# Kernel optimization log

Measured on AMD Instinct MI355X. Metric: run time of the kernel, lower is better.

## Reference

```python
import jax, jax.numpy as jnp
import numpy as np
from itertools import combinations_with_replacement

LATENT_DIM = 16
N_PARAMS = 2
N_VARS = LATENT_DIM + N_PARAMS  # 18
POLY_ORDER = 3
BATCH = 131072

# Static exponent index tables: for each degree d, an [n_terms_d, d] array of
# variable indices (combinations with replacement), matching a sympy-style
# polynomial library [1, x_i, x_i*x_j, x_i*x_j*x_k, ...].
IDX = [np.array(list(combinations_with_replacement(range(N_VARS), d)), dtype=np.int32)
       for d in range(1, POLY_ORDER + 1)]
P = 1 + sum(a.shape[0] for a in IDX)  # 1330 library terms


def setup_inputs() -> dict:
    key = jax.random.key(0)
    k1, k2, k3 = jax.random.split(key, 3)
    z = jax.random.normal(k1, (BATCH, LATENT_DIM), dtype=jnp.float32)
    betas = jax.random.normal(k2, (BATCH, N_PARAMS), dtype=jnp.float32)
    big_xi = jax.random.normal(k3, (P, N_VARS), dtype=jnp.float32) * 0.1
    mask = jnp.ones((P, N_VARS), dtype=jnp.float32)
    return {"z": z, "betas": betas, "big_xi": big_xi, "mask": mask}


def _theta(x):
    # x: [B, N_VARS] -> theta: [B, P]
    cols = [jnp.ones((x.shape[0], 1), dtype=x.dtype)]  # constant term
    for idx in IDX:
        acc = x[:, idx[:, 0]]                # [B, n_terms_d]
        for k in range(1, idx.shape[1]):     # loop over degree (<= POLY_ORDER)
            acc = acc * x[:, idx[:, k]]
        cols.append(acc)
    return jnp.concatenate(cols, axis=1)


def reference(z, betas, big_xi, mask):
    x = jnp.concatenate([z, betas], axis=1)  # [B, N_VARS]
    theta = _theta(x)                        # [B, P]
    return theta @ (big_xi * mask)           # [B, N_VARS]
```

## Files before the change

kernel.cpp:

```cpp
#include <hip/hip_runtime.h>
#include <hip/hip_bf16.h>
#include <utility>


constexpr int NVARS   = 18;
constexpr int NOUT    = 18;
constexpr int NROWS   = 131072;
constexpr int NCHUNKS = 43;
constexpr int NSLOTS  = NCHUNKS * 8;

constexpr int WF0_SHORTS = NCHUNKS * 512;
constexpr int WF1_SHORTS = NCHUNKS * 72;
constexpr int WF_SHORTS  = WF0_SHORTS + WF1_SHORTS;

typedef __attribute__((ext_vector_type(8))) short short8;
typedef __attribute__((ext_vector_type(4))) float f32x4;

struct T3 { int a, b, c; };

constexpr int rho1(int v) {
    if (v < 16)  return (v & ~3) | ((v + 1) & 3);
    if (v == 16) return 17;
    if (v == 17) return 16;
    return v;
}
constexpr int rho2v(int v) { return rho1(rho1(v)); }

constexpr T3 sort3(int u0, int u1, int u2) {
    int t = 0;
    if (u0 > u1) { t = u0; u0 = u1; u1 = t; }
    if (u1 > u2) { t = u1; u1 = u2; u2 = t; }
    if (u0 > u1) { t = u0; u0 = u1; u1 = t; }
    return T3{u0, u1, u2};
}
constexpr T3 rho3(T3 t) { return sort3(rho1(t.a), rho1(t.b), rho1(t.c)); }

constexpr bool t3_less(T3 x, T3 y) {
    if (x.a != y.a) return x.a < y.a;
    if (x.b != y.b) return x.b < y.b;
    return x.c < y.c;
}
constexpr bool t3_eq(T3 x, T3 y) { return x.a == y.a && x.b == y.b && x.c == y.c; }

constexpr int rank_of(T3 t) {
    int deg = (t.a < 18) + (t.b < 18) + (t.c < 18);
    if (deg == 0) return 0;
    if (deg == 1) return 1 + t.a;
    if (deg == 2) {
        int r = 19;
        for (int a = 0; a < t.a; ++a) r += 18 - a;
        return r + (t.b - t.a);
    }
    int r = 190;
    for (int a = 0; a < t.a; ++a) { int n = 18 - a; r += n * (n + 1) / 2; }
    for (int b = t.a; b < t.b; ++b) r += 18 - b;
    return r + (t.c - t.b);
}

struct RepTables {
    signed char va[NSLOTS], vb[NSLOTS], vc[NSLOTS];
    short p[4][NSLOTS];
    int count;
};

constexpr void consider(RepTables& R, int& s, T3 t) {
    T3 im[4] = {t, T3{0, 0, 0}, T3{0, 0, 0}, T3{0, 0, 0}};
    im[1] = rho3(im[0]);
    im[2] = rho3(im[1]);
    im[3] = rho3(im[2]);
    for (int g = 1; g < 4; ++g)
        if (t3_less(im[g], t)) return;
    R.va[s] = (signed char)t.a; R.vb[s] = (signed char)t.b; R.vc[s] = (signed char)t.c;
    for (int g = 0; g < 4; ++g) {
        bool dup = false;
        for (int h = 0; h < g; ++h)
            if (t3_eq(im[h], im[g])) dup = true;
        R.p[g][s] = dup ? (short)-1 : (short)rank_of(im[g]);
    }
    ++s;
}

constexpr RepTables make_tables() {
    RepTables R{};
    int s = 0;
    consider(R, s, T3{18, 18, 18});
    for (int a = 0; a < NVARS; ++a) consider(R, s, T3{a, 18, 18});
    for (int a = 0; a < NVARS; ++a)
        for (int b = a; b < NVARS; ++b) consider(R, s, T3{a, b, 18});
    for (int a = 0; a < NVARS; ++a)
        for (int b = a; b < NVARS; ++b)
            for (int c = b; c < NVARS; ++c) consider(R, s, T3{a, b, c});
    R.count = s;
    for (; s < NSLOTS; ++s) {
        R.va[s] = 19; R.vb[s] = 19; R.vc[s] = 19;
        for (int g = 0; g < 4; ++g) R.p[g][s] = -1;
    }
    return R;
}

constexpr RepTables h_tab = make_tables();
static_assert(h_tab.count == 342, "orbit enumeration must give 342 rep slots");
__device__ const RepTables d_tab = make_tables();

__device__ __align__(16) short g_wf[WF_SHORTS];


#if __has_builtin(__builtin_amdgcn_cvt_pk_bf16_f32)
typedef __bf16 bf16x2 __attribute__((ext_vector_type(2)));
__device__ __forceinline__ unsigned pack2(float f0, float f1) {
    bf16x2 r = __builtin_amdgcn_cvt_pk_bf16_f32(f0, f1);
    return __builtin_bit_cast(unsigned, r);
}
#else
__device__ __forceinline__ unsigned pack2(float f0, float f1) {
    unsigned u0 = __float_as_uint(f0) + 0x8000u;
    unsigned u1 = __float_as_uint(f1) + 0x8000u;
    return __builtin_amdgcn_perm(u1, u0, 0x07060302u);
}
#endif


template <int S>
__device__ __forceinline__ float term_val(const float (&x)[NVARS]) {
    constexpr int a = h_tab.va[S], b = h_tab.vb[S], c = h_tab.vc[S];
    if constexpr (a >= 19)      return 0.0f;
    else if constexpr (a == 18) return 1.0f;
    else if constexpr (b == 18) return x[a];
    else if constexpr (c == 18) return x[a] * x[b];
    else                        return x[a] * x[b] * x[c];
}

union AFrag { unsigned u[4]; short8 v; };

template <int CI, int... I>
__device__ __forceinline__ void eval8(const float (&x)[NVARS], float (&t)[8],
                                      std::integer_sequence<int, I...>) {
    ((t[I] = term_val<CI * 8 + I>(x)), ...);
}

template <int CI>
__device__ __forceinline__ void kstep(const float (&x)[NVARS],
                                      const short* p0, const short* p1,
                                      f32x4& acc0, f32x4& acc1) {
    float t[8];
    eval8<CI>(x, t, std::make_integer_sequence<int, 8>{});
    AFrag af;
#pragma unroll
    for (int j = 0; j < 4; ++j) af.u[j] = pack2(t[2 * j], t[2 * j + 1]);
    short8 b0 = *(const short8*)(p0 + CI * 512);
    short8 b1 = *(const short8*)(p1 + CI * 72);
    acc0 = __builtin_amdgcn_mfma_f32_16x16x32_bf16(af.v, b0, acc0, 0, 0, 0);
    acc1 = __builtin_amdgcn_mfma_f32_16x16x32_bf16(af.v, b1, acc1, 0, 0, 0);
}

template <int... CI>
__device__ __forceinline__ void kloop(const float (&x)[NVARS],
                                      const short* p0, const short* p1,
                                      f32x4& acc0, f32x4& acc1,
                                      std::integer_sequence<int, CI...>) {
    (kstep<CI>(x, p0, p1, acc0, acc1), ...);
}

__device__ __forceinline__ void load_x(const float* __restrict__ z,
                                       const float* __restrict__ betas,
                                       int arow, bool s1, bool s2, float (&x)[NVARS]) {
    float x0[NVARS];
    const float4* z4 = (const float4*)(z + (size_t)arow * 16);
    float4 v0 = z4[0], v1 = z4[1], v2 = z4[2], v3 = z4[3];
    x0[0]  = v0.x; x0[1]  = v0.y; x0[2]  = v0.z; x0[3]  = v0.w;
    x0[4]  = v1.x; x0[5]  = v1.y; x0[6]  = v1.z; x0[7]  = v1.w;
    x0[8]  = v2.x; x0[9]  = v2.y; x0[10] = v2.z; x0[11] = v2.w;
    x0[12] = v3.x; x0[13] = v3.y; x0[14] = v3.z; x0[15] = v3.w;
    const float2 b2 = *(const float2*)(betas + (size_t)arow * 2);
    x0[16] = b2.x; x0[17] = b2.y;
    float y[NVARS];
#pragma unroll
    for (int v = 0; v < NVARS; ++v) y[v] = s1 ? x0[rho1(v)] : x0[v];
#pragma unroll
    for (int v = 0; v < NVARS; ++v) x[v] = s2 ? y[rho2v(v)] : y[v];
}

__global__ __launch_bounds__(512, 4) void vindy_mfma(const float* __restrict__ z,
                                                     const float* __restrict__ betas,
                                                     float* __restrict__ out) {
    __shared__ __align__(16) short ldsW[WF_SHORTS];

    {
        const float4* src = (const float4*)g_wf;
        float4* dst = (float4*)ldsW;
        for (int i = threadIdx.x; i < WF_SHORTS / 8; i += 512) dst[i] = src[i];
    }
    __syncthreads();

    const int lane = threadIdx.x & 63;
    const int wave = threadIdx.x >> 6;
    const int g    = lane >> 4;
    const int n    = lane & 15;
    const int row0 = blockIdx.x * 128 + wave * 16;

    const bool s1 = (g & 1) != 0;
    const bool s2 = (g & 2) != 0;
    float x[NVARS];
    load_x(z, betas, row0 + n, s1, s2, x);

    const short* p0 = ldsW + lane * 8;
    const short* p1 = ldsW + WF0_SHORTS + (n < 2 ? (g * 2 + n) * 8 : 64);

    f32x4 acc0, acc1;
#pragma unroll
    for (int i = 0; i < 4; ++i) { acc0[i] = 0.0f; acc1[i] = 0.0f; }

    kloop(x, p0, p1, acc0, acc1, std::make_integer_sequence<int, NCHUNKS>{});

    float* o = out + (size_t)(row0 + g * 4) * NOUT;
#pragma unroll
    for (int r = 0; r < 4; ++r) o[(size_t)r * NOUT + n] = acc0[r];
    if (n < 2) {
#pragma unroll
        for (int r = 0; r < 4; ++r) o[(size_t)r * NOUT + 16 + n] = acc1[r];
    }
}


__global__ void prep_wfrag(const float* __restrict__ xi, const float* __restrict__ mask) {
    int i = blockIdx.x * blockDim.x + threadIdx.x;
    if (i >= WF_SHORTS) return;
    float v = 0.0f;
    if (i < WF0_SHORTS) {
        int j = i & 7, l = (i >> 3) & 63, c = i >> 9;
        int col = l & 15;
        int p = d_tab.p[l >> 4][c * 8 + j];
        if (p >= 0) v = xi[p * NOUT + col] * mask[p * NOUT + col];
    } else {
        int i2 = i - WF0_SHORTS;
        int c = i2 / 72;
        int r = i2 - c * 72;
        int q = r >> 3, j = r & 7;
        if (q < 8) {
            int col = 16 + (q & 1);
            int p = d_tab.p[q >> 1][c * 8 + j];
            if (p >= 0) v = xi[p * NOUT + col] * mask[p * NOUT + col];
        }
    }
    g_wf[i] = __builtin_bit_cast(short, __float2bfloat16(v));
}

extern "C" void kernel_launch(void* const* d_in, const int* in_sizes, int n_in,
                              void* d_out, int out_size, void* d_ws, size_t ws_size,
                              hipStream_t stream) {
    const float* z     = (const float*)d_in[0];
    const float* betas = (const float*)d_in[1];
    const float* xi    = (const float*)d_in[2];
    const float* mask  = (const float*)d_in[3];
    float* out = (float*)d_out;
    (void)d_ws; (void)ws_size;

    prep_wfrag<<<(WF_SHORTS + 255) / 256, 256, 0, stream>>>(xi, mask);
    vindy_mfma<<<NROWS / 128, 512, 0, stream>>>(z, betas, out);
}
```

Baseline: 89.37 us.

## Switch to 32x32x16 MFMA covering all 18 outputs in one accumulator

Replaces the pair of 16x16x32 MFMAs (one for 16 output columns, one mostly-idle one for the last 2) with a single 32x32x16 MFMA per chunk whose 32 columns cover all 18 outputs. Lanes are split into two halves with a single permutation, and the second orbit permutation is handled by a second pass of 43 chunks over the same rows. The weight fragment layout in LDS is rebuilt with a 304-short chunk stride, and each block now processes 256 rows. The aim is to drop the redundant second MFMA and reuse the term evaluation across more output columns, at the cost of 14 unused columns per MFMA and roughly double the term evaluations per lane.

```diff
diff --git a/kernel.cpp b/kernel.cpp
--- a/kernel.cpp
+++ b/kernel.cpp
@@ -9,12 +9,12 @@
 constexpr int NCHUNKS = 43;
 constexpr int NSLOTS  = NCHUNKS * 8;
 
-constexpr int WF0_SHORTS = NCHUNKS * 512;
-constexpr int WF1_SHORTS = NCHUNKS * 72;
-constexpr int WF_SHORTS  = WF0_SHORTS + WF1_SHORTS;
-
-typedef __attribute__((ext_vector_type(8))) short short8;
-typedef __attribute__((ext_vector_type(4))) float f32x4;
+constexpr int CH_STRIDE = 304;
+constexpr int WF2_SHORTS = 86 * CH_STRIDE;
+constexpr int LDS_SHORTS = 32768;
+
+typedef __attribute__((ext_vector_type(8)))  short short8;
+typedef __attribute__((ext_vector_type(16))) float f32x16;
 
 struct T3 { int a, b, c; };
 
@@ -102,7 +102,7 @@
 static_assert(h_tab.count == 342, "orbit enumeration must give 342 rep slots");
 __device__ const RepTables d_tab = make_tables();
 
-__device__ __align__(16) short g_wf[WF_SHORTS];
+__device__ __align__(16) short g_wf2[WF2_SHORTS];
 
 
 #if __has_builtin(__builtin_amdgcn_cvt_pk_bf16_f32)
@@ -132,38 +132,32 @@
 
 union AFrag { unsigned u[4]; short8 v; };
 
-template <int CI, int... I>
-__device__ __forceinline__ void eval8(const float (&x)[NVARS], float (&t)[8],
-                                      std::integer_sequence<int, I...>) {
-    ((t[I] = term_val<CI * 8 + I>(x)), ...);
+template <int S, int... J>
+__device__ __forceinline__ void pack8(const float (&x)[NVARS], AFrag& af,
+                                      std::integer_sequence<int, J...>) {
+    ((af.u[J] = pack2(term_val<S + 2 * J>(x), term_val<S + 2 * J + 1>(x))), ...);
 }
 
 template <int CI>
-__device__ __forceinline__ void kstep(const float (&x)[NVARS],
-                                      const short* p0, const short* p1,
-                                      f32x4& acc0, f32x4& acc1) {
-    float t[8];
-    eval8<CI>(x, t, std::make_integer_sequence<int, 8>{});
+__device__ __forceinline__ void kstep32(const float (&x)[NVARS],
+                                        const short* pB, f32x16& acc) {
+    constexpr int S = (CI < 43 ? CI : CI - 43) * 8;
     AFrag af;
-#pragma unroll
-    for (int j = 0; j < 4; ++j) af.u[j] = pack2(t[2 * j], t[2 * j + 1]);
-    short8 b0 = *(const short8*)(p0 + CI * 512);
-    short8 b1 = *(const short8*)(p1 + CI * 72);
-    acc0 = __builtin_amdgcn_mfma_f32_16x16x32_bf16(af.v, b0, acc0, 0, 0, 0);
-    acc1 = __builtin_amdgcn_mfma_f32_16x16x32_bf16(af.v, b1, acc1, 0, 0, 0);
-}
-
-template <int... CI>
-__device__ __forceinline__ void kloop(const float (&x)[NVARS],
-                                      const short* p0, const short* p1,
-                                      f32x4& acc0, f32x4& acc1,
-                                      std::integer_sequence<int, CI...>) {
-    (kstep<CI>(x, p0, p1, acc0, acc1), ...);
+    pack8<S>(x, af, std::make_integer_sequence<int, 4>{});
+    short8 b = *(const short8*)(pB + CI * CH_STRIDE);
+    acc = __builtin_amdgcn_mfma_f32_32x32x16_bf16(af.v, b, acc, 0, 0, 0);
+}
+
+template <int BASE, int... CI>
+__device__ __forceinline__ void kloop32(const float (&x)[NVARS],
+                                        const short* pB, f32x16& acc,
+                                        std::integer_sequence<int, CI...>) {
+    (kstep32<BASE + CI>(x, pB, acc), ...);
 }
 
 __device__ __forceinline__ void load_x(const float* __restrict__ z,
                                        const float* __restrict__ betas,
-                                       int arow, bool s1, bool s2, float (&x)[NVARS]) {
+                                       int arow, bool s1, float (&x)[NVARS]) {
     float x0[NVARS];
     const float4* z4 = (const float4*)(z + (size_t)arow * 16);
     float4 v0 = z4[0], v1 = z4[1], v2 = z4[2], v3 = z4[3];
@@ -173,76 +167,75 @@
     x0[12] = v3.x; x0[13] = v3.y; x0[14] = v3.z; x0[15] = v3.w;
     const float2 b2 = *(const float2*)(betas + (size_t)arow * 2);
     x0[16] = b2.x; x0[17] = b2.y;
-    float y[NVARS];
-#pragma unroll
-    for (int v = 0; v < NVARS; ++v) y[v] = s1 ? x0[rho1(v)] : x0[v];
-#pragma unroll
-    for (int v = 0; v < NVARS; ++v) x[v] = s2 ? y[rho2v(v)] : y[v];
+#pragma unroll
+    for (int v = 0; v < NVARS; ++v) x[v] = s1 ? x0[rho1(v)] : x0[v];
 }
 
 __global__ __launch_bounds__(512, 4) void vindy_mfma(const float* __restrict__ z,
                                                      const float* __restrict__ betas,
                                                      float* __restrict__ out) {
-    __shared__ __align__(16) short ldsW[WF_SHORTS];
+    __shared__ __align__(16) short ldsW[LDS_SHORTS];
 
     {
-        const float4* src = (const float4*)g_wf;
+        const float4* src = (const float4*)g_wf2;
         float4* dst = (float4*)ldsW;
-        for (int i = threadIdx.x; i < WF_SHORTS / 8; i += 512) dst[i] = src[i];
+        for (int i = threadIdx.x; i < WF2_SHORTS / 8; i += 512) dst[i] = src[i];
     }
     __syncthreads();
 
     const int lane = threadIdx.x & 63;
     const int wave = threadIdx.x >> 6;
-    const int g    = lane >> 4;
-    const int n    = lane & 15;
-    const int row0 = blockIdx.x * 128 + wave * 16;
-
-    const bool s1 = (g & 1) != 0;
-    const bool s2 = (g & 2) != 0;
-    float x[NVARS];
-    load_x(z, betas, row0 + n, s1, s2, x);
-
-    const short* p0 = ldsW + lane * 8;
-    const short* p1 = ldsW + WF0_SHORTS + (n < 2 ? (g * 2 + n) * 8 : 64);
-
-    f32x4 acc0, acc1;
-#pragma unroll
-    for (int i = 0; i < 4; ++i) { acc0[i] = 0.0f; acc1[i] = 0.0f; }
-
-    kloop(x, p0, p1, acc0, acc1, std::make_integer_sequence<int, NCHUNKS>{});
-
-    float* o = out + (size_t)(row0 + g * 4) * NOUT;
-#pragma unroll
-    for (int r = 0; r < 4; ++r) o[(size_t)r * NOUT + n] = acc0[r];
-    if (n < 2) {
-#pragma unroll
-        for (int r = 0; r < 4; ++r) o[(size_t)r * NOUT + 16 + n] = acc1[r];
+    const int h    = lane >> 5;
+    const int col  = lane & 31;
+    const int row0 = blockIdx.x * 256 + wave * 32;
+
+    float x1[NVARS];
+    load_x(z, betas, row0 + col, h != 0, x1);
+
+    const int col_eff = (col < NOUT) ? col : NOUT;
+    const short* pB = ldsW + h * 152 + col_eff * 8;
+
+    f32x16 acc;
+#pragma unroll
+    for (int i = 0; i < 16; ++i) acc[i] = 0.0f;
+
+    kloop32<0>(x1, pB, acc, std::make_integer_sequence<int, 43>{});
+
+    float x2[NVARS];
+#pragma unroll
+    for (int v = 0; v < NVARS; ++v) x2[v] = x1[rho2v(v)];
+
+    kloop32<43>(x2, pB, acc, std::make_integer_sequence<int, 43>{});
+
+    if (col < NOUT) {
+#pragma unroll
+        for (int q = 0; q < 4; ++q) {
+#pragma unroll
+            for (int r = 0; r < 4; ++r) {
+                int row = r + 8 * q + 4 * h;
+                out[(size_t)(row0 + row) * NOUT + col] = acc[q * 4 + r];
+            }
+        }
     }
 }
 
 
 __global__ void prep_wfrag(const float* __restrict__ xi, const float* __restrict__ mask) {
     int i = blockIdx.x * blockDim.x + threadIdx.x;
-    if (i >= WF_SHORTS) return;
+    if (i >= WF2_SHORTS) return;
+    int c  = i / CH_STRIDE;
+    int r  = i - c * CH_STRIDE;
+    int h  = r / 152;
+    int r2 = r - h * 152;
+    int col = r2 >> 3, j = r2 & 7;
     float v = 0.0f;
-    if (i < WF0_SHORTS) {
-        int j = i & 7, l = (i >> 3) & 63, c = i >> 9;
-        int col = l & 15;
-        int p = d_tab.p[l >> 4][c * 8 + j];
+    if (col < NOUT) {
+        int g = (c < 43 ? 0 : 2) + h;
+        int s = (c < 43 ? c : c - 43) * 8 + j;
+        int p = d_tab.p[g][s];
         if (p >= 0) v = xi[p * NOUT + col] * mask[p * NOUT + col];
-    } else {
-        int i2 = i - WF0_SHORTS;
-        int c = i2 / 72;
-        int r = i2 - c * 72;
-        int q = r >> 3, j = r & 7;
-        if (q < 8) {
-            int col = 16 + (q & 1);
-            int p = d_tab.p[q >> 1][c * 8 + j];
-            if (p >= 0) v = xi[p * NOUT + col] * mask[p * NOUT + col];
-        }
-    }
-    g_wf[i] = __builtin_bit_cast(short, __float2bfloat16(v));
+    }
+    g_wf2[i] = __builtin_bit_cast(short, __float2bfloat16(v));
 }
 
 extern "C" void kernel_launch(void* const* d_in, const int* in_sizes, int n_in,
@@ -255,6 +248,6 @@
     float* out = (float*)d_out;
     (void)d_ws; (void)ws_size;
 
-    prep_wfrag<<<(WF_SHORTS + 255) / 256, 256, 0, stream>>>(xi, mask);
-    vindy_mfma<<<NROWS / 128, 512, 0, stream>>>(z, betas, out);
-}
+    prep_wfrag<<<(WF2_SHORTS + 255) / 256, 256, 0, stream>>>(xi, mask);
+    vindy_mfma<<<NROWS / 256, 512, 0, stream>>>(z, betas, out);
+}
```

After: 86.04 us, median of 3. 3.7% less time.
